# Kernel optimization log

Hardware: AMD Instinct MI355X
Metric: run time of the kernel (lower is better)

The kernel has to match this reference:

```python
import jax, jax.numpy as jnp
import numpy as np

MAX_DISP = 4  # matches init_kwargs max_displacement


def setup_inputs() -> dict:
    key = jax.random.key(0)
    k1, k2 = jax.random.split(key)
    B, C, H, W = 8, 256, 128, 128
    in1 = jax.random.normal(k1, (B, C, H, W), dtype=jnp.float32)
    in2 = jax.random.normal(k2, (B, C, H, W), dtype=jnp.float32)
    return {"in1": in1, "in2": in2}


def reference(in1, in2):
    d = MAX_DISP
    B, C, H, W = in1.shape
    # zero-pad in2 by d on both spatial dims (ConstantPad2d(d, 0))
    in2_pad = jnp.pad(in2, ((0, 0), (0, 0), (d, d), (d, d)))
    # torch.meshgrid default 'ij' indexing + reshape(-1): dy varies slow, dx fast
    outs = [
        jnp.sum(in1 * jax.lax.dynamic_slice(in2_pad, (0, 0, dy, dx), (B, C, H, W)), axis=1)
        for dy in range(2 * d + 1)
        for dx in range(2 * d + 1)
    ]
    return jnp.stack(outs, axis=1)  # [B, (2d+1)^2, H, W]
```

## Files before the change

kernel.cpp:

```cpp
#include <hip/hip_runtime.h>


constexpr int Bn = 8, Cn = 256, Hn = 128, Wn = 128, HW = Hn * Wn;
constexpr int Dd = 4, ND = 9;
constexpr int KC = 16;
constexpr int NP = KC / 2;
constexpr int NT = 576;
constexpr int W2 = Wn + 8;

typedef __fp16 h2v __attribute__((ext_vector_type(2)));

static __device__ __forceinline__ unsigned packh2(float a, float b) {
  h2v h = __builtin_amdgcn_cvt_pkrtz(a, b);
  return __builtin_bit_cast(unsigned, h);
}

static __device__ __forceinline__ float dot2(unsigned a, unsigned b, float c) {
#if __has_builtin(__builtin_amdgcn_fdot2)
  return __builtin_amdgcn_fdot2(__builtin_bit_cast(h2v, a),
                                __builtin_bit_cast(h2v, b), c, false);
#else
  h2v ha = __builtin_bit_cast(h2v, a), hb = __builtin_bit_cast(h2v, b);
  return c + (float)ha.x * (float)hb.x + (float)ha.y * (float)hb.y;
#endif
}

__global__ __launch_bounds__(NT) void corr_kernel(
    const float* __restrict__ in1, const float* __restrict__ in2,
    float* __restrict__ out)
{
  __shared__ __align__(16) unsigned s1h[NP][2][Wn];
  __shared__ __align__(16) unsigned s2h[NP][10][W2];

  int bid = blockIdx.x;
  bid = (bid & 7) * 64 + (bid >> 3);
  const int b  = bid >> 6;
  const int y0 = (bid & 63) << 1;

  const int tid  = threadIdx.x;
  const int dy   = tid >> 6;
  const int lane = tid & 63;
  const int row  = lane >> 5;
  const int xq   = (lane & 31) << 2;

  const size_t base = (size_t)b * Cn * HW;

  for (int i = tid * 4; i < NP * 10 * W2; i += NT * 4)
    *(uint4*)(&s2h[0][0][0] + i) = uint4{0, 0, 0, 0};

  float4 acc[ND];
#pragma unroll
  for (int dx = 0; dx < ND; ++dx) acc[dx] = float4{0.f, 0.f, 0.f, 0.f};

  const int srow = dy + row;

  for (int c0 = 0; c0 < Cn; c0 += KC) {
    __syncthreads();

    for (int i = tid; i < NP * 2 * 32; i += NT) {
      const int p  = i >> 6;
      const int yy = (i >> 5) & 1;
      const int gx = (i & 31) << 2;
      const float* s = in1 + base + (size_t)(c0 + 2 * p) * HW + (y0 + yy) * Wn + gx;
      const float4 f0 = *(const float4*)s;
      const float4 f1 = *(const float4*)(s + HW);
      uint4 w;
      w.x = packh2(f0.x, f1.x); w.y = packh2(f0.y, f1.y);
      w.z = packh2(f0.z, f1.z); w.w = packh2(f0.w, f1.w);
      *(uint4*)&s1h[p][yy][gx] = w;
    }

    for (int i = tid; i < NP * 10 * 32; i += NT) {
      const int p   = i / 320;
      const int rem = i - p * 320;
      const int r   = rem >> 5;
      const int gx  = (rem & 31) << 2;
      const int gy  = y0 + r - Dd;
      const bool ok = (unsigned)gy < (unsigned)Hn;
      const int gyc = ok ? gy : 0;
      const float* s = in2 + base + (size_t)(c0 + 2 * p) * HW + (size_t)gyc * Wn + gx;
      const float4 f0 = *(const float4*)s;
      const float4 f1 = *(const float4*)(s + HW);
      uint4 w;
      w.x = packh2(f0.x, f1.x); w.y = packh2(f0.y, f1.y);
      w.z = packh2(f0.z, f1.z); w.w = packh2(f0.w, f1.w);
      if (!ok) w = uint4{0, 0, 0, 0};
      *(uint4*)&s2h[p][r][4 + gx] = w;
    }
    __syncthreads();

#pragma unroll
    for (int kc = 0; kc < NP; ++kc) {
      const unsigned* bp = &s2h[kc][srow][xq];
      const uint4 b0 = *(const uint4*)bp;
      const uint4 b1 = *(const uint4*)(bp + 4);
      const uint4 b2 = *(const uint4*)(bp + 8);
      const uint4 av = *(const uint4*)&s1h[kc][row][xq];
      const unsigned bb[12] = {b0.x, b0.y, b0.z, b0.w, b1.x, b1.y,
                               b1.z, b1.w, b2.x, b2.y, b2.z, b2.w};
      const unsigned aa[4] = {av.x, av.y, av.z, av.w};
#pragma unroll
      for (int dx = 0; dx < ND; ++dx) {
        acc[dx].x = dot2(aa[0], bb[0 + dx], acc[dx].x);
        acc[dx].y = dot2(aa[1], bb[1 + dx], acc[dx].y);
        acc[dx].z = dot2(aa[2], bb[2 + dx], acc[dx].z);
        acc[dx].w = dot2(aa[3], bb[3 + dx], acc[dx].w);
      }
    }
  }

#pragma unroll
  for (int dx = 0; dx < ND; ++dx) {
    const size_t o =
        (((size_t)b * (ND * ND) + dy * ND + dx) * Hn + (y0 + row)) * Wn + xq;
    *(float4*)&out[o] = acc[dx];
  }
}

extern "C" void kernel_launch(void* const* d_in, const int* in_sizes, int n_in,
                              void* d_out, int out_size, void* d_ws, size_t ws_size,
                              hipStream_t stream) {
  const float* in1 = (const float*)d_in[0];
  const float* in2 = (const float*)d_in[1];
  float* out = (float*)d_out;
  dim3 grid(Bn * (Hn / 2));
  dim3 block(NT);
  hipLaunchKernelGGL(corr_kernel, grid, block, 0, stream, in1, in2, out);
}
```

Before: 111.0 us.

## Double-buffer LDS staging with register prefetch of next channel chunk

Rewrites the channel loop so each chunk's global loads go into registers before the compute on the current LDS buffer, then are packed into the other LDS buffer after compute. There is now one barrier per iteration instead of two. The chunk size drops from 16 to 8 channels so two buffers fit, and address computation is hoisted into per-thread precomputed pointers with only the halo columns zeroed. The intent is to hide global load latency behind the dot-product work, at the cost of more registers and twice as many loop iterations.

```diff
diff --git a/kernel.cpp b/kernel.cpp
--- a/kernel.cpp
+++ b/kernel.cpp
@@ -3,10 +3,14 @@
 
 constexpr int Bn = 8, Cn = 256, Hn = 128, Wn = 128, HW = Hn * Wn;
 constexpr int Dd = 4, ND = 9;
-constexpr int KC = 16;
-constexpr int NP = KC / 2;
+constexpr int KC = 8, NP = KC / 2;
+constexpr int NCH = Cn / KC;
 constexpr int NT = 576;
 constexpr int W2 = Wn + 8;
+constexpr int S1SZ = NP * 2 * Wn;
+constexpr int S2SZ = NP * 10 * W2;
+constexpr int BUF  = S1SZ + S2SZ;
+constexpr int KCHW = KC * HW;
 
 typedef __fp16 h2v __attribute__((ext_vector_type(2)));
 
@@ -29,8 +33,7 @@
     const float* __restrict__ in1, const float* __restrict__ in2,
     float* __restrict__ out)
 {
-  __shared__ __align__(16) unsigned s1h[NP][2][Wn];
-  __shared__ __align__(16) unsigned s2h[NP][10][W2];
+  __shared__ __align__(16) unsigned lds[2 * BUF];
 
   int bid = blockIdx.x;
   bid = (bid & 7) * 64 + (bid >> 3);
@@ -42,71 +45,103 @@
   const int lane = tid & 63;
   const int row  = lane >> 5;
   const int xq   = (lane & 31) << 2;
-
+  const int srow = dy + row;
   const size_t base = (size_t)b * Cn * HW;
 
-  for (int i = tid * 4; i < NP * 10 * W2; i += NT * 4)
-    *(uint4*)(&s2h[0][0][0] + i) = uint4{0, 0, 0, 0};
+  const bool stager = tid < 512;
+  const float* src[3]; int dst[3]; bool ok[3];
+#pragma unroll
+  for (int s = 0; s < 3; ++s) {
+    const int g = (tid & 511) + s * 512;
+    if (g < 256) {
+      const int p = g >> 6, yy = (g >> 5) & 1, gx = (g & 31) << 2;
+      src[s] = in1 + base + (size_t)(2 * p) * HW + (y0 + yy) * Wn + gx;
+      dst[s] = p * (2 * Wn) + yy * Wn + gx;
+      ok[s]  = true;
+    } else {
+      const int g2 = g - 256;
+      const int p = g2 / 320, rem = g2 - p * 320;
+      const int r = rem >> 5, gx = (rem & 31) << 2;
+      const int gy = y0 + r - Dd;
+      ok[s] = (unsigned)gy < (unsigned)Hn;
+      src[s] = in2 + base + (size_t)(2 * p) * HW + (size_t)(ok[s] ? gy : 0) * Wn + gx;
+      dst[s] = S1SZ + (p * 10 + r) * W2 + 4 + gx;
+    }
+  }
+
+  for (int i = tid; i < 2 * NP * 10 * 2; i += NT) {
+    const int bh = i / (NP * 10 * 2), rem = i - bh * (NP * 10 * 2);
+    const int pr = rem >> 1, side = rem & 1;
+    *(uint4*)&lds[bh * BUF + S1SZ + pr * W2 + side * 132] = uint4{0, 0, 0, 0};
+  }
+
+  float4 pre[3][2];
+  if (stager) {
+#pragma unroll
+    for (int s = 0; s < 3; ++s) {
+      pre[s][0] = *(const float4*)src[s];
+      pre[s][1] = *(const float4*)(src[s] + HW);
+    }
+#pragma unroll
+    for (int s = 0; s < 3; ++s) {
+      uint4 w;
+      w.x = packh2(pre[s][0].x, pre[s][1].x); w.y = packh2(pre[s][0].y, pre[s][1].y);
+      w.z = packh2(pre[s][0].z, pre[s][1].z); w.w = packh2(pre[s][0].w, pre[s][1].w);
+      if (!ok[s]) w = uint4{0, 0, 0, 0};
+      *(uint4*)&lds[dst[s]] = w;
+    }
+  }
+  __syncthreads();
 
   float4 acc[ND];
 #pragma unroll
   for (int dx = 0; dx < ND; ++dx) acc[dx] = float4{0.f, 0.f, 0.f, 0.f};
 
-  const int srow = dy + row;
+  for (int c = 0; c < NCH; ++c) {
+    const int  cur  = c & 1;
+    const bool more = (c + 1) < NCH;
 
-  for (int c0 = 0; c0 < Cn; c0 += KC) {
-    __syncthreads();
-
-    for (int i = tid; i < NP * 2 * 32; i += NT) {
-      const int p  = i >> 6;
-      const int yy = (i >> 5) & 1;
-      const int gx = (i & 31) << 2;
-      const float* s = in1 + base + (size_t)(c0 + 2 * p) * HW + (y0 + yy) * Wn + gx;
-      const float4 f0 = *(const float4*)s;
-      const float4 f1 = *(const float4*)(s + HW);
-      uint4 w;
-      w.x = packh2(f0.x, f1.x); w.y = packh2(f0.y, f1.y);
-      w.z = packh2(f0.z, f1.z); w.w = packh2(f0.w, f1.w);
-      *(uint4*)&s1h[p][yy][gx] = w;
+    if (more && stager) {
+      const size_t ofs = (size_t)(c + 1) * KCHW;
+#pragma unroll
+      for (int s = 0; s < 3; ++s) {
+        pre[s][0] = *(const float4*)(src[s] + ofs);
+        pre[s][1] = *(const float4*)(src[s] + ofs + HW);
+      }
     }
 
-    for (int i = tid; i < NP * 10 * 32; i += NT) {
-      const int p   = i / 320;
-      const int rem = i - p * 320;
-      const int r   = rem >> 5;
-      const int gx  = (rem & 31) << 2;
-      const int gy  = y0 + r - Dd;
-      const bool ok = (unsigned)gy < (unsigned)Hn;
-      const int gyc = ok ? gy : 0;
-      const float* s = in2 + base + (size_t)(c0 + 2 * p) * HW + (size_t)gyc * Wn + gx;
-      const float4 f0 = *(const float4*)s;
-      const float4 f1 = *(const float4*)(s + HW);
-      uint4 w;
-      w.x = packh2(f0.x, f1.x); w.y = packh2(f0.y, f1.y);
-      w.z = packh2(f0.z, f1.z); w.w = packh2(f0.w, f1.w);
-      if (!ok) w = uint4{0, 0, 0, 0};
-      *(uint4*)&s2h[p][r][4 + gx] = w;
-    }
-    __syncthreads();
-
+    const unsigned* bufp = &lds[cur * BUF];
 #pragma unroll
     for (int kc = 0; kc < NP; ++kc) {
-      const unsigned* bp = &s2h[kc][srow][xq];
+      const uint4 av = *(const uint4*)(bufp + kc * (2 * Wn) + row * Wn + xq);
+      const unsigned* bp = bufp + S1SZ + (kc * 10 + srow) * W2 + xq;
       const uint4 b0 = *(const uint4*)bp;
       const uint4 b1 = *(const uint4*)(bp + 4);
       const uint4 b2 = *(const uint4*)(bp + 8);
-      const uint4 av = *(const uint4*)&s1h[kc][row][xq];
+      const unsigned aa[4]  = {av.x, av.y, av.z, av.w};
       const unsigned bb[12] = {b0.x, b0.y, b0.z, b0.w, b1.x, b1.y,
                                b1.z, b1.w, b2.x, b2.y, b2.z, b2.w};
-      const unsigned aa[4] = {av.x, av.y, av.z, av.w};
 #pragma unroll
       for (int dx = 0; dx < ND; ++dx) {
-        acc[dx].x = dot2(aa[0], bb[0 + dx], acc[dx].x);
-        acc[dx].y = dot2(aa[1], bb[1 + dx], acc[dx].y);
-        acc[dx].z = dot2(aa[2], bb[2 + dx], acc[dx].z);
-        acc[dx].w = dot2(aa[3], bb[3 + dx], acc[dx].w);
+        acc[dx].x = dot2(aa[0], bb[dx + 0], acc[dx].x);
+        acc[dx].y = dot2(aa[1], bb[dx + 1], acc[dx].y);
+        acc[dx].z = dot2(aa[2], bb[dx + 2], acc[dx].z);
+        acc[dx].w = dot2(aa[3], bb[dx + 3], acc[dx].w);
       }
     }
+
+    if (more && stager) {
+      const int nb = (cur ^ 1) * BUF;
+#pragma unroll
+      for (int s = 0; s < 3; ++s) {
+        uint4 w;
+        w.x = packh2(pre[s][0].x, pre[s][1].x); w.y = packh2(pre[s][0].y, pre[s][1].y);
+        w.z = packh2(pre[s][0].z, pre[s][1].z); w.w = packh2(pre[s][0].w, pre[s][1].w);
+        if (!ok[s]) w = uint4{0, 0, 0, 0};
+        *(uint4*)&lds[nb + dst[s]] = w;
+      }
+    }
+    __syncthreads();
   }
 
 #pragma unroll
```

New measurement: 111.8 us. Within noise of the previous version (+0.7%).

## Split each block's row tile into two column halves to double grid size

Applied to the files above, without the earlier changes.

Each block now handles a 64-column half of a two-row tile instead of the full width, which doubles the grid from 512 to 1024 blocks. Each thread computes two output pixels per displacement instead of four. The in2 halo columns are loaded from the neighbouring half or zero-filled at the image edge, and the two staging loops are merged into one. The aim is more blocks in flight across the CUs, at the cost of extra halo loads, higher LDS/load overhead per output and a branchier staging loop.

```diff
diff --git a/kernel.cpp b/kernel.cpp
--- a/kernel.cpp
+++ b/kernel.cpp
@@ -3,10 +3,13 @@
 
 constexpr int Bn = 8, Cn = 256, Hn = 128, Wn = 128, HW = Hn * Wn;
 constexpr int Dd = 4, ND = 9;
-constexpr int KC = 16;
-constexpr int NP = KC / 2;
+constexpr int KC = 16, NP = KC / 2;
 constexpr int NT = 576;
-constexpr int W2 = Wn + 8;
+constexpr int XW = 64;
+constexpr int W2 = XW + 8;
+constexpr int NG1 = NP * 2 * (XW / 4);
+constexpr int NG2 = NP * 10 * 17;
+constexpr int NG  = NG1 + NG2;
 
 typedef __fp16 h2v __attribute__((ext_vector_type(2)));
 
@@ -29,82 +32,86 @@
     const float* __restrict__ in1, const float* __restrict__ in2,
     float* __restrict__ out)
 {
-  __shared__ __align__(16) unsigned s1h[NP][2][Wn];
+  __shared__ __align__(16) unsigned s1h[NP][2][XW];
   __shared__ __align__(16) unsigned s2h[NP][10][W2];
 
   int bid = blockIdx.x;
-  bid = (bid & 7) * 64 + (bid >> 3);
-  const int b  = bid >> 6;
-  const int y0 = (bid & 63) << 1;
+  bid = (bid & 7) * 128 + (bid >> 3);
+  const int b     = bid >> 7;
+  const int yp    = (bid >> 1) & 63;
+  const int xh    = bid & 1;
+  const int y0    = yp << 1;
+  const int xbase = xh << 6;
 
   const int tid  = threadIdx.x;
   const int dy   = tid >> 6;
   const int lane = tid & 63;
   const int row  = lane >> 5;
-  const int xq   = (lane & 31) << 2;
-
+  const int x0   = (lane & 31) << 1;
+  const int srow = dy + row;
   const size_t base = (size_t)b * Cn * HW;
 
-  for (int i = tid * 4; i < NP * 10 * W2; i += NT * 4)
-    *(uint4*)(&s2h[0][0][0] + i) = uint4{0, 0, 0, 0};
+  for (int i = tid; i < NP * 10; i += NT) {
+    const int p = i / 10, r = i - p * 10;
+    *(uint4*)&s2h[p][r][xh ? 68 : 0] = uint4{0, 0, 0, 0};
+  }
 
-  float4 acc[ND];
+  float2 acc[ND];
 #pragma unroll
-  for (int dx = 0; dx < ND; ++dx) acc[dx] = float4{0.f, 0.f, 0.f, 0.f};
-
-  const int srow = dy + row;
+  for (int dx = 0; dx < ND; ++dx) acc[dx] = float2{0.f, 0.f};
 
   for (int c0 = 0; c0 < Cn; c0 += KC) {
     __syncthreads();
 
-    for (int i = tid; i < NP * 2 * 32; i += NT) {
-      const int p  = i >> 6;
-      const int yy = (i >> 5) & 1;
-      const int gx = (i & 31) << 2;
-      const float* s = in1 + base + (size_t)(c0 + 2 * p) * HW + (y0 + yy) * Wn + gx;
-      const float4 f0 = *(const float4*)s;
-      const float4 f1 = *(const float4*)(s + HW);
-      uint4 w;
-      w.x = packh2(f0.x, f1.x); w.y = packh2(f0.y, f1.y);
-      w.z = packh2(f0.z, f1.z); w.w = packh2(f0.w, f1.w);
-      *(uint4*)&s1h[p][yy][gx] = w;
-    }
-
-    for (int i = tid; i < NP * 10 * 32; i += NT) {
-      const int p   = i / 320;
-      const int rem = i - p * 320;
-      const int r   = rem >> 5;
-      const int gx  = (rem & 31) << 2;
-      const int gy  = y0 + r - Dd;
-      const bool ok = (unsigned)gy < (unsigned)Hn;
-      const int gyc = ok ? gy : 0;
-      const float* s = in2 + base + (size_t)(c0 + 2 * p) * HW + (size_t)gyc * Wn + gx;
-      const float4 f0 = *(const float4*)s;
-      const float4 f1 = *(const float4*)(s + HW);
-      uint4 w;
-      w.x = packh2(f0.x, f1.x); w.y = packh2(f0.y, f1.y);
-      w.z = packh2(f0.z, f1.z); w.w = packh2(f0.w, f1.w);
-      if (!ok) w = uint4{0, 0, 0, 0};
-      *(uint4*)&s2h[p][r][4 + gx] = w;
+    for (int i = tid; i < NG; i += NT) {
+      if (i < NG1) {
+        const int p = i >> 5, yy = (i >> 4) & 1, q = i & 15;
+        const float* s =
+            in1 + base + (size_t)(c0 + 2 * p) * HW + (y0 + yy) * Wn + xbase + (q << 2);
+        const float4 f0 = *(const float4*)s;
+        const float4 f1 = *(const float4*)(s + HW);
+        uint4 w;
+        w.x = packh2(f0.x, f1.x); w.y = packh2(f0.y, f1.y);
+        w.z = packh2(f0.z, f1.z); w.w = packh2(f0.w, f1.w);
+        *(uint4*)&s1h[p][yy][q << 2] = w;
+      } else {
+        int g = i - NG1;
+        const int p = g / 170; g -= p * 170;
+        const int r = g / 17;
+        const int q = g - r * 17;
+        const int gy = y0 + r - Dd;
+        const bool ok = (unsigned)gy < (unsigned)Hn;
+        int dstx, gx;
+        if (q < 16) { dstx = 4 + (q << 2); gx = xbase + (q << 2); }
+        else {
+          dstx = xh ? 0 : 68;
+          gx   = xh ? (xbase - 4) : (xbase + 64);
+        }
+        const float* s =
+            in2 + base + (size_t)(c0 + 2 * p) * HW + (size_t)(ok ? gy : 0) * Wn + gx;
+        const float4 f0 = *(const float4*)s;
+        const float4 f1 = *(const float4*)(s + HW);
+        uint4 w;
+        w.x = packh2(f0.x, f1.x); w.y = packh2(f0.y, f1.y);
+        w.z = packh2(f0.z, f1.z); w.w = packh2(f0.w, f1.w);
+        if (!ok) w = uint4{0, 0, 0, 0};
+        *(uint4*)&s2h[p][r][dstx] = w;
+      }
     }
     __syncthreads();
 
 #pragma unroll
     for (int kc = 0; kc < NP; ++kc) {
-      const unsigned* bp = &s2h[kc][srow][xq];
-      const uint4 b0 = *(const uint4*)bp;
-      const uint4 b1 = *(const uint4*)(bp + 4);
-      const uint4 b2 = *(const uint4*)(bp + 8);
-      const uint4 av = *(const uint4*)&s1h[kc][row][xq];
-      const unsigned bb[12] = {b0.x, b0.y, b0.z, b0.w, b1.x, b1.y,
-                               b1.z, b1.w, b2.x, b2.y, b2.z, b2.w};
-      const unsigned aa[4] = {av.x, av.y, av.z, av.w};
+      const uint2 aa = *(const uint2*)&s1h[kc][row][x0];
+      const unsigned* bp = &s2h[kc][srow][x0];
+      unsigned bb[10];
+#pragma unroll
+      for (int j = 0; j < 5; ++j)
+        *(uint2*)&bb[2 * j] = *(const uint2*)(bp + 2 * j);
 #pragma unroll
       for (int dx = 0; dx < ND; ++dx) {
-        acc[dx].x = dot2(aa[0], bb[0 + dx], acc[dx].x);
-        acc[dx].y = dot2(aa[1], bb[1 + dx], acc[dx].y);
-        acc[dx].z = dot2(aa[2], bb[2 + dx], acc[dx].z);
-        acc[dx].w = dot2(aa[3], bb[3 + dx], acc[dx].w);
+        acc[dx].x = dot2(aa.x, bb[dx], acc[dx].x);
+        acc[dx].y = dot2(aa.y, bb[dx + 1], acc[dx].y);
       }
     }
   }
@@ -112,8 +119,8 @@
 #pragma unroll
   for (int dx = 0; dx < ND; ++dx) {
     const size_t o =
-        (((size_t)b * (ND * ND) + dy * ND + dx) * Hn + (y0 + row)) * Wn + xq;
-    *(float4*)&out[o] = acc[dx];
+        (((size_t)b * (ND * ND) + dy * ND + dx) * Hn + (y0 + row)) * Wn + xbase + x0;
+    *(float2*)&out[o] = acc[dx];
   }
 }
 
@@ -123,7 +130,7 @@
   const float* in1 = (const float*)d_in[0];
   const float* in2 = (const float*)d_in[1];
   float* out = (float*)d_out;
-  dim3 grid(Bn * (Hn / 2));
+  dim3 grid(Bn * (Hn / 2) * 2);
   dim3 block(NT);
   hipLaunchKernelGGL(corr_kernel, grid, block, 0, stream, in1, in2, out);
 }
```

New measurement: 164.5 us. 1.48x slower.

## Split dy range across three blocks and read in1 directly from global

Applied to the files above, without the earlier changes.

Each block now covers one pair of output rows and a third of the vertical displacements (3 dy values), which triples the grid and shrinks blocks to 192 threads with an occupancy hint. The in2 shared tile shrinks to 4 rows and only its padding columns are zeroed. in1 is no longer staged in shared memory: each thread loads and packs its own in1 values from global inside the compute loop. This aims for more blocks in flight and less shared memory per block, at the cost of reading in1 and in2 rows redundantly across the three dy-group blocks.

```diff
diff --git a/kernel.cpp b/kernel.cpp
--- a/kernel.cpp
+++ b/kernel.cpp
@@ -3,9 +3,9 @@
 
 constexpr int Bn = 8, Cn = 256, Hn = 128, Wn = 128, HW = Hn * Wn;
 constexpr int Dd = 4, ND = 9;
-constexpr int KC = 16;
-constexpr int NP = KC / 2;
-constexpr int NT = 576;
+constexpr int KC = 16, NP = KC / 2;
+constexpr int NT = 192;
+constexpr int NR = 4;
 constexpr int W2 = Wn + 8;
 
 typedef __fp16 h2v __attribute__((ext_vector_type(2)));
@@ -25,86 +25,80 @@
 #endif
 }
 
-__global__ __launch_bounds__(NT) void corr_kernel(
+__global__ __launch_bounds__(NT, 7) void corr_kernel(
     const float* __restrict__ in1, const float* __restrict__ in2,
     float* __restrict__ out)
 {
-  __shared__ __align__(16) unsigned s1h[NP][2][Wn];
-  __shared__ __align__(16) unsigned s2h[NP][10][W2];
+  __shared__ __align__(16) unsigned s2h[NP][NR][W2];
 
   int bid = blockIdx.x;
-  bid = (bid & 7) * 64 + (bid >> 3);
-  const int b  = bid >> 6;
-  const int y0 = (bid & 63) << 1;
+  bid = (bid & 7) * 192 + (bid >> 3);
+  const int b   = bid / 192;
+  int rem = bid - b * 192;
+  const int yp  = rem / 3;
+  const int dyg = rem - yp * 3;
+  const int y0  = yp << 1;
 
   const int tid  = threadIdx.x;
-  const int dy   = tid >> 6;
+  const int wv   = tid >> 6;
+  const int dy   = dyg * 3 + wv;
   const int lane = tid & 63;
   const int row  = lane >> 5;
-  const int xq   = (lane & 31) << 2;
-
+  const int x0   = (lane & 31) << 2;
+  const int rr   = wv + row;
   const size_t base = (size_t)b * Cn * HW;
 
-  for (int i = tid * 4; i < NP * 10 * W2; i += NT * 4)
-    *(uint4*)(&s2h[0][0][0] + i) = uint4{0, 0, 0, 0};
+  for (int i = tid; i < NP * NR * 2; i += NT) {
+    const int p = i >> 3, r = (i >> 1) & 3, side = i & 1;
+    *(uint4*)&s2h[p][r][side ? 132 : 0] = uint4{0, 0, 0, 0};
+  }
 
   float4 acc[ND];
 #pragma unroll
   for (int dx = 0; dx < ND; ++dx) acc[dx] = float4{0.f, 0.f, 0.f, 0.f};
 
-  const int srow = dy + row;
+  const float* in1p = in1 + base + (size_t)(y0 + row) * Wn + x0;
 
   for (int c0 = 0; c0 < Cn; c0 += KC) {
     __syncthreads();
 
-    for (int i = tid; i < NP * 2 * 32; i += NT) {
-      const int p  = i >> 6;
-      const int yy = (i >> 5) & 1;
-      const int gx = (i & 31) << 2;
-      const float* s = in1 + base + (size_t)(c0 + 2 * p) * HW + (y0 + yy) * Wn + gx;
-      const float4 f0 = *(const float4*)s;
-      const float4 f1 = *(const float4*)(s + HW);
-      uint4 w;
-      w.x = packh2(f0.x, f1.x); w.y = packh2(f0.y, f1.y);
-      w.z = packh2(f0.z, f1.z); w.w = packh2(f0.w, f1.w);
-      *(uint4*)&s1h[p][yy][gx] = w;
-    }
-
-    for (int i = tid; i < NP * 10 * 32; i += NT) {
-      const int p   = i / 320;
-      const int rem = i - p * 320;
-      const int r   = rem >> 5;
-      const int gx  = (rem & 31) << 2;
-      const int gy  = y0 + r - Dd;
+    for (int g = tid; g < NP * NR * 32; g += NT) {
+      const int p = g >> 7;
+      const int r = (g >> 5) & 3;
+      const int q = g & 31;
+      const int gy = y0 + dyg * 3 + r - Dd;
       const bool ok = (unsigned)gy < (unsigned)Hn;
-      const int gyc = ok ? gy : 0;
-      const float* s = in2 + base + (size_t)(c0 + 2 * p) * HW + (size_t)gyc * Wn + gx;
+      const float* s = in2 + base + (size_t)(c0 + 2 * p) * HW +
+                       (size_t)(ok ? gy : 0) * Wn + (q << 2);
       const float4 f0 = *(const float4*)s;
       const float4 f1 = *(const float4*)(s + HW);
       uint4 w;
       w.x = packh2(f0.x, f1.x); w.y = packh2(f0.y, f1.y);
       w.z = packh2(f0.z, f1.z); w.w = packh2(f0.w, f1.w);
       if (!ok) w = uint4{0, 0, 0, 0};
-      *(uint4*)&s2h[p][r][4 + gx] = w;
+      *(uint4*)&s2h[p][r][(q << 2) + 4] = w;
     }
     __syncthreads();
 
+    const float* ip = in1p + (size_t)c0 * HW;
 #pragma unroll
-    for (int kc = 0; kc < NP; ++kc) {
-      const unsigned* bp = &s2h[kc][srow][xq];
+    for (int p = 0; p < NP; ++p) {
+      const float4 f0 = *(const float4*)(ip + (size_t)(2 * p) * HW);
+      const float4 f1 = *(const float4*)(ip + (size_t)(2 * p + 1) * HW);
+      const unsigned aa[4] = {packh2(f0.x, f1.x), packh2(f0.y, f1.y),
+                              packh2(f0.z, f1.z), packh2(f0.w, f1.w)};
+      const unsigned* bp = &s2h[p][rr][x0];
       const uint4 b0 = *(const uint4*)bp;
       const uint4 b1 = *(const uint4*)(bp + 4);
       const uint4 b2 = *(const uint4*)(bp + 8);
-      const uint4 av = *(const uint4*)&s1h[kc][row][xq];
       const unsigned bb[12] = {b0.x, b0.y, b0.z, b0.w, b1.x, b1.y,
                                b1.z, b1.w, b2.x, b2.y, b2.z, b2.w};
-      const unsigned aa[4] = {av.x, av.y, av.z, av.w};
 #pragma unroll
       for (int dx = 0; dx < ND; ++dx) {
-        acc[dx].x = dot2(aa[0], bb[0 + dx], acc[dx].x);
-        acc[dx].y = dot2(aa[1], bb[1 + dx], acc[dx].y);
-        acc[dx].z = dot2(aa[2], bb[2 + dx], acc[dx].z);
-        acc[dx].w = dot2(aa[3], bb[3 + dx], acc[dx].w);
+        acc[dx].x = dot2(aa[0], bb[dx + 0], acc[dx].x);
+        acc[dx].y = dot2(aa[1], bb[dx + 1], acc[dx].y);
+        acc[dx].z = dot2(aa[2], bb[dx + 2], acc[dx].z);
+        acc[dx].w = dot2(aa[3], bb[dx + 3], acc[dx].w);
       }
     }
   }
@@ -112,7 +106,7 @@
 #pragma unroll
   for (int dx = 0; dx < ND; ++dx) {
     const size_t o =
-        (((size_t)b * (ND * ND) + dy * ND + dx) * Hn + (y0 + row)) * Wn + xq;
+        (((size_t)b * (ND * ND) + dy * ND + dx) * Hn + (y0 + row)) * Wn + x0;
     *(float4*)&out[o] = acc[dx];
   }
 }
@@ -123,7 +117,7 @@
   const float* in1 = (const float*)d_in[0];
   const float* in2 = (const float*)d_in[1];
   float* out = (float*)d_out;
-  dim3 grid(Bn * (Hn / 2));
+  dim3 grid(Bn * (Hn / 2) * 3);
   dim3 block(NT);
   hipLaunchKernelGGL(corr_kernel, grid, block, 0, stream, in1, in2, out);
 }
```

Measured after the change: 151.2 us. 36.2% more time.
